# Kernel optimization log

Measured on AMD Instinct MI355X. Metric: run time of the kernel, lower is better.

The kernel has to match this reference:

```python
import jax, jax.numpy as jnp
import numpy as np

B, C, H, W = 4, 128, 64, 64
CQ = C // 8  # query/key channels = 16


def setup_inputs() -> dict:
    key = jax.random.key(0)
    ks = jax.random.split(key, 8)
    s = 0.05
    return {
        "x": jax.random.normal(ks[0], (B, C, H, W), jnp.float32),
        "wq": jax.random.normal(ks[1], (CQ, C), jnp.float32) * s,
        "bq": jax.random.normal(ks[2], (CQ,), jnp.float32) * s,
        "wk": jax.random.normal(ks[3], (CQ, C), jnp.float32) * s,
        "bk": jax.random.normal(ks[4], (CQ,), jnp.float32) * s,
        "wv": jax.random.normal(ks[5], (C, C), jnp.float32) * s,
        "bv": jax.random.normal(ks[6], (C,), jnp.float32) * s,
        # original inits gamma to 0; use small nonzero so attention path is exercised
        "gamma": jax.random.normal(ks[7], (1,), jnp.float32) * 0.1,
    }


def reference(x, wq, bq, wk, bk, wv, bv, gamma):
    b, c, h, w = x.shape
    n = h * w
    xf = x.reshape(b, c, n)  # [B, C, N]
    # 1x1 convs are per-position linear maps over channels
    q = jnp.einsum("qc,bcn->bnq", wq, xf) + bq            # [B, N, Cq]
    k = jnp.einsum("qc,bcn->bqn", wk, xf) + bk[:, None]   # [B, Cq, N]
    v = jnp.einsum("oc,bcn->bon", wv, xf) + bv[:, None]   # [B, C, N]
    # unscaled scores, softmax over keys (last dim), as in the original
    attn = jax.nn.softmax(jnp.einsum("bnq,bqm->bnm", q, k), axis=-1)  # [B, N, N]
    # out = value @ attention^T : out[b,c,n] = sum_m v[b,c,m] * attn[b,n,m]
    out = jnp.einsum("bom,bnm->bon", v, attn)             # [B, C, N]
    return gamma[0] * out.reshape(b, c, h, w) + x
```

## Files before the change

kernel.cpp:

```cpp
#include <hip/hip_runtime.h>
#include <hip/hip_bf16.h>

typedef float f32x4  __attribute__((ext_vector_type(4)));
typedef float f32x16 __attribute__((ext_vector_type(16)));
typedef short s16x8  __attribute__((ext_vector_type(8)));

#define NB 4
#define NC 128
#define NNPOS 4096
#define KSP 4
#define QBLK 128

__device__ __forceinline__ short bf16s(float x) {
    __hip_bfloat16 h = __float2bfloat16(x);
    return *reinterpret_cast<short*>(&h);
}
__device__ __forceinline__ int packbf2(float lo, float hi) {
    __hip_bfloat162 t = __float22bfloat162_rn(float2{lo, hi});
    return *reinterpret_cast<int*>(&t);
}
__device__ __forceinline__ float bf2f(unsigned short u) {
    unsigned int v = ((unsigned int)u) << 16;
    return *reinterpret_cast<float*>(&v);
}

__global__ __launch_bounds__(256) void qkv_kernel(
    const float* __restrict__ x,
    const float* __restrict__ wq, const float* __restrict__ bq,
    const float* __restrict__ wk, const float* __restrict__ bk,
    const float* __restrict__ wv, const float* __restrict__ bv,
    short* __restrict__ qb, short* __restrict__ kb, short* __restrict__ vt)
{
    const int n0  = blockIdx.x * 32;
    const int b   = blockIdx.y;
    const int tid = threadIdx.x;
    const int w = tid >> 6, lane = tid & 63, quad = lane >> 4, nn = lane & 15;

    __shared__ __align__(16) short xsT[32 * 136];

    #pragma unroll
    for (int p = 0; p < 4; ++p) {
        int idx = tid + p * 256;
        int cc = idx >> 3, n4 = (idx & 7) * 4;
        f32x4 xv = *(const f32x4*)&x[((size_t)(b * NC + cc)) * NNPOS + n0 + n4];
        #pragma unroll
        for (int j = 0; j < 4; ++j)
            xsT[(n4 + j) * 136 + cc] = bf16s(xv[j]);
    }

    s16x8 af[3][4];
    bool  live[3];
    f32x4 biasv[3];
    #pragma unroll
    for (int t = 0; t < 3; ++t) {
        int rid = 3 * w + t;
        int R   = rid * 16;
        const float* wsrc = nullptr; const float* bsrc = nullptr; int row0 = 0;
        if (rid < 8)        { wsrc = wv; bsrc = bv; row0 = R; }
        else if (rid == 8)  { wsrc = wq; bsrc = bq; row0 = 0; }
        else if (rid == 10) { wsrc = wk; bsrc = bk; row0 = 0; }
        live[t] = (wsrc != nullptr);
        #pragma unroll
        for (int r = 0; r < 4; ++r)
            biasv[t][r] = live[t] ? bsrc[row0 + quad * 4 + r] : 0.0f;
        if (live[t]) {
            #pragma unroll
            for (int ks = 0; ks < 4; ++ks) {
                const float* src = wsrc + (size_t)(row0 + nn) * NC + ks * 32 + quad * 8;
                f32x4 wa = *(const f32x4*)src;
                f32x4 wb = *(const f32x4*)(src + 4);
                s16x8 f;
                #pragma unroll
                for (int j = 0; j < 4; ++j) { f[j] = bf16s(wa[j]); f[j + 4] = bf16s(wb[j]); }
                af[t][ks] = f;
            }
        }
    }
    __syncthreads();

    f32x4 acc[3][2];
    #pragma unroll
    for (int t = 0; t < 3; ++t)
        #pragma unroll
        for (int nt = 0; nt < 2; ++nt)
            acc[t][nt] = biasv[t];

    #pragma unroll
    for (int nt = 0; nt < 2; ++nt) {
        s16x8 bf[4];
        #pragma unroll
        for (int ks = 0; ks < 4; ++ks)
            bf[ks] = *(const s16x8*)&xsT[(nt * 16 + nn) * 136 + ks * 32 + quad * 8];
        #pragma unroll
        for (int t = 0; t < 3; ++t)
            if (live[t])
                #pragma unroll
                for (int ks = 0; ks < 4; ++ks)
                    acc[t][nt] = __builtin_amdgcn_mfma_f32_16x16x32_bf16(af[t][ks], bf[ks], acc[t][nt], 0, 0, 0);
    }

    #pragma unroll
    for (int t = 0; t < 3; ++t) {
        if (!live[t]) continue;
        int R = (3 * w + t) * 16;
        #pragma unroll
        for (int nt = 0; nt < 2; ++nt) {
            int n = n0 + nt * 16 + nn;
            #pragma unroll
            for (int r = 0; r < 4; ++r) {
                short v = bf16s(acc[t][nt][r]);
                int row = R + quad * 4 + r;
                if (row < 128)
                    vt[((size_t)(b * NC + row)) * NNPOS + n] = v;
                else if (row < 144)
                    qb[((size_t)(b * NNPOS) + n) * 16 + (row - 128)] = v;
                else
                    kb[((size_t)(b * NNPOS) + n) * 16 + (row - 160)] = v;
            }
        }
    }
}

__global__ __launch_bounds__(256, 2) void attn_kernel(
    const short* __restrict__ qb, const short* __restrict__ kb,
    const short* __restrict__ vt,
    unsigned short* __restrict__ Ow, float* __restrict__ lw)
{
    const int qblk = blockIdx.x;
    const int s    = blockIdx.y;
    const int b    = blockIdx.z;
    const int tid  = threadIdx.x;
    const int w = tid >> 6, lane = tid & 63, h = lane >> 5, c31 = lane & 31;

    __shared__ __align__(16) short vts[128 * 72];

    const int q0 = qblk * QBLK + w * 32;

    s16x8 bq = *(const s16x8*)(qb + ((size_t)(b * NNPOS) + q0 + c31) * 16 + h * 8);

    f32x16 acc[4];
    #pragma unroll
    for (int ct = 0; ct < 4; ++ct)
        #pragma unroll
        for (int r = 0; r < 16; ++r) acc[ct][r] = 0.0f;
    float lp = 0.0f;

    const int mbase = s * (NNPOS / KSP);

    for (int it = 0; it < (NNPOS / KSP) / 64; ++it) {
        const int m0 = mbase + it * 64;

        s16x8 ak0 = *(const s16x8*)(kb + ((size_t)(b * NNPOS) + m0      + c31) * 16 + h * 8);
        s16x8 ak1 = *(const s16x8*)(kb + ((size_t)(b * NNPOS) + m0 + 32 + c31) * 16 + h * 8);

        __syncthreads();
        #pragma unroll
        for (int p = 0; p < 4; ++p) {
            int idx = tid + p * 256;
            int cc = idx >> 3, jq = idx & 7;
            *(uint4*)(vts + cc * 72 + jq * 8) =
                *(const uint4*)(vt + ((size_t)(b * NC + cc)) * NNPOS + m0 + jq * 8);
        }

        f32x16 z;
        #pragma unroll
        for (int r = 0; r < 16; ++r) z[r] = 0.0f;
        f32x16 s0 = __builtin_amdgcn_mfma_f32_32x32x16_bf16(ak0, bq, z, 0, 0, 0);
        f32x16 s1 = __builtin_amdgcn_mfma_f32_32x32x16_bf16(ak1, bq, z, 0, 0, 0);

        int d[16];
        #pragma unroll
        for (int i = 0; i < 8; ++i) {
            float p0 = __expf(fminf(s0[2 * i], 80.f));
            float p1 = __expf(fminf(s0[2 * i + 1], 80.f));
            lp += p0 + p1;
            d[i] = packbf2(p0, p1);
        }
        #pragma unroll
        for (int i = 0; i < 8; ++i) {
            float p0 = __expf(fminf(s1[2 * i], 80.f));
            float p1 = __expf(fminf(s1[2 * i + 1], 80.f));
            lp += p0 + p1;
            d[8 + i] = packbf2(p0, p1);
        }
        int xw[16];
        #pragma unroll
        for (int i = 0; i < 16; ++i) xw[i] = __shfl_xor(d[i], 32, 64);

        s16x8 pa[4];
        #pragma unroll
        for (int kp = 0; kp < 4; ++kp) {
            int e = kp * 4;
            union { int i[4]; s16x8 v; } u;
            u.i[0] = h ? xw[e + 2] : d[e];
            u.i[1] = h ? xw[e + 3] : d[e + 1];
            u.i[2] = h ? d[e + 2]  : xw[e];
            u.i[3] = h ? d[e + 3]  : xw[e + 1];
            pa[kp] = u.v;
        }

        __syncthreads();
        #pragma unroll
        for (int kp = 0; kp < 4; ++kp)
            #pragma unroll
            for (int ct = 0; ct < 4; ++ct) {
                s16x8 bv = *(const s16x8*)(vts + (ct * 32 + c31) * 72 + kp * 16 + h * 8);
                acc[ct] = __builtin_amdgcn_mfma_f32_32x32x16_bf16(pa[kp], bv, acc[ct], 0, 0, 0);
            }
    }

    lp += __shfl_xor(lp, 32, 64);
    if (lane < 32)
        lw[((size_t)(b * KSP + s)) * NNPOS + q0 + c31] = lp;

    #pragma unroll
    for (int ct = 0; ct < 4; ++ct)
        #pragma unroll
        for (int r = 0; r < 16; ++r) {
            int q = q0 + (r & 3) + 8 * (r >> 2) + 4 * h;
            Ow[(((size_t)(b * KSP + s)) * NNPOS + q) * NC + ct * 32 + c31] =
                (unsigned short)bf16s(acc[ct][r]);
        }
}

__global__ __launch_bounds__(256) void combine_kernel(
    const unsigned short* __restrict__ Ow, const float* __restrict__ lw,
    const float* __restrict__ x, const float* __restrict__ gamma,
    float* __restrict__ out)
{
    const int n0  = blockIdx.x * 64;
    const int b   = blockIdx.y;
    const int tid = threadIdx.x;

    __shared__ float ot[128 * 65 + 64];
    float* lsum = ot + 128 * 65;

    if (tid < 64) {
        float sl = 0.f;
        #pragma unroll
        for (int sI = 0; sI < KSP; ++sI)
            sl += lw[((size_t)(b * KSP + sI)) * NNPOS + n0 + tid];
        lsum[tid] = sl;
    }
    __syncthreads();

    #pragma unroll
    for (int p = 0; p < 16; ++p) {
        int e = tid + p * 256;
        int cp = e & 63, n = e >> 6;
        float a0 = 0.f, a1 = 0.f;
        #pragma unroll
        for (int sI = 0; sI < KSP; ++sI) {
            const unsigned short* src = Ow +
                (((size_t)(b * KSP + sI)) * NNPOS + n0 + n) * NC + cp * 2;
            ushort2 u = *(const ushort2*)src;
            a0 += bf2f(u.x);
            a1 += bf2f(u.y);
        }
        float inv = 1.0f / lsum[n];
        ot[(cp * 2) * 65 + n]     = a0 * inv;
        ot[(cp * 2 + 1) * 65 + n] = a1 * inv;
    }
    __syncthreads();

    const float g = gamma[0];
    #pragma unroll
    for (int p = 0; p < 32; ++p) {
        int e = tid + p * 256;
        int n = e & 63, c = e >> 6;
        size_t a = ((size_t)(b * NC + c)) * NNPOS + n0 + n;
        out[a] = g * ot[c * 65 + n] + x[a];
    }
}

extern "C" void kernel_launch(void* const* d_in, const int* in_sizes, int n_in,
                              void* d_out, int out_size, void* d_ws, size_t ws_size,
                              hipStream_t stream) {
    const float* x     = (const float*)d_in[0];
    const float* wq    = (const float*)d_in[1];
    const float* bq    = (const float*)d_in[2];
    const float* wk    = (const float*)d_in[3];
    const float* bk    = (const float*)d_in[4];
    const float* wv    = (const float*)d_in[5];
    const float* bv    = (const float*)d_in[6];
    const float* gamma = (const float*)d_in[7];
    float* out = (float*)d_out;

    short* qb = (short*)d_ws;
    short* kb = qb + (size_t)NB * NNPOS * 16;
    short* vt = kb + (size_t)NB * NNPOS * 16;
    unsigned short* Ow = (unsigned short*)(vt + (size_t)NB * NC * NNPOS);
    float* lw = (float*)(Ow + (size_t)NB * KSP * NNPOS * NC);

    qkv_kernel<<<dim3(128, NB), 256, 0, stream>>>(x, wq, bq, wk, bk, wv, bv, qb, kb, vt);
    attn_kernel<<<dim3(NNPOS / QBLK, KSP, NB), 256, 0, stream>>>(qb, kb, vt, Ow, lw);
    combine_kernel<<<dim3(NNPOS / 64, NB), 256, 0, stream>>>(Ow, lw, x, gamma, out);
}
```

Baseline: 122.3 us.

## Register-tile two query tiles per wave and load V directly from global

The attention kernel now has each wave handle 64 queries as two 32-row tiles, so every V fragment feeds two MFMAs. The shared-memory staging of V and both block barriers are removed, and V fragments are read straight from global memory into registers in two halves. The key-split count doubles and the query block doubles, which keeps the grid size the same but doubles the partial outputs the combine kernel must read. Accumulator register pressure doubles, which may cut occupancy or cause spills.

```diff
diff --git a/kernel.cpp b/kernel.cpp
--- a/kernel.cpp
+++ b/kernel.cpp
@@ -8,8 +8,8 @@
 #define NB 4
 #define NC 128
 #define NNPOS 4096
-#define KSP 4
-#define QBLK 128
+#define KSP 8
+#define QBLK 256
 
 __device__ __forceinline__ short bf16s(float x) {
     __hip_bfloat16 h = __float2bfloat16(x);
@@ -132,20 +132,22 @@
     const int tid  = threadIdx.x;
     const int w = tid >> 6, lane = tid & 63, h = lane >> 5, c31 = lane & 31;
 
-    __shared__ __align__(16) short vts[128 * 72];
-
-    const int q0 = qblk * QBLK + w * 32;
-
-    s16x8 bq = *(const s16x8*)(qb + ((size_t)(b * NNPOS) + q0 + c31) * 16 + h * 8);
-
-    f32x16 acc[4];
-    #pragma unroll
-    for (int ct = 0; ct < 4; ++ct)
-        #pragma unroll
-        for (int r = 0; r < 16; ++r) acc[ct][r] = 0.0f;
-    float lp = 0.0f;
+    const int q0 = qblk * QBLK + w * 64;
+
+    s16x8 bq0 = *(const s16x8*)(qb + ((size_t)(b * NNPOS) + q0      + c31) * 16 + h * 8);
+    s16x8 bq1 = *(const s16x8*)(qb + ((size_t)(b * NNPOS) + q0 + 32 + c31) * 16 + h * 8);
+
+    f32x16 acc[2][4];
+    #pragma unroll
+    for (int qt = 0; qt < 2; ++qt)
+        #pragma unroll
+        for (int ct = 0; ct < 4; ++ct)
+            #pragma unroll
+            for (int r = 0; r < 16; ++r) acc[qt][ct][r] = 0.0f;
+    float lp[2] = {0.f, 0.f};
 
     const int mbase = s * (NNPOS / KSP);
+    const short* vbase = vt + (size_t)(b * NC) * NNPOS;
 
     for (int it = 0; it < (NNPOS / KSP) / 64; ++it) {
         const int m0 = mbase + it * 64;
@@ -153,74 +155,96 @@
         s16x8 ak0 = *(const s16x8*)(kb + ((size_t)(b * NNPOS) + m0      + c31) * 16 + h * 8);
         s16x8 ak1 = *(const s16x8*)(kb + ((size_t)(b * NNPOS) + m0 + 32 + c31) * 16 + h * 8);
 
-        __syncthreads();
-        #pragma unroll
-        for (int p = 0; p < 4; ++p) {
-            int idx = tid + p * 256;
-            int cc = idx >> 3, jq = idx & 7;
-            *(uint4*)(vts + cc * 72 + jq * 8) =
-                *(const uint4*)(vt + ((size_t)(b * NC + cc)) * NNPOS + m0 + jq * 8);
+        s16x8 vb0[4][2];
+        #pragma unroll
+        for (int ct = 0; ct < 4; ++ct)
+            #pragma unroll
+            for (int k2 = 0; k2 < 2; ++k2)
+                vb0[ct][k2] = *(const s16x8*)(vbase +
+                    (size_t)(ct * 32 + c31) * NNPOS + m0 + k2 * 16 + h * 8);
+
+        s16x8 pa[2][4];
+        #pragma unroll
+        for (int qt = 0; qt < 2; ++qt) {
+            s16x8 bqt = qt ? bq1 : bq0;
+            f32x16 z;
+            #pragma unroll
+            for (int r = 0; r < 16; ++r) z[r] = 0.0f;
+            f32x16 s0 = __builtin_amdgcn_mfma_f32_32x32x16_bf16(ak0, bqt, z, 0, 0, 0);
+            f32x16 s1 = __builtin_amdgcn_mfma_f32_32x32x16_bf16(ak1, bqt, z, 0, 0, 0);
+            int d[16];
+            #pragma unroll
+            for (int i = 0; i < 8; ++i) {
+                float p0 = __expf(fminf(s0[2 * i], 80.f));
+                float p1 = __expf(fminf(s0[2 * i + 1], 80.f));
+                lp[qt] += p0 + p1;
+                d[i] = packbf2(p0, p1);
+            }
+            #pragma unroll
+            for (int i = 0; i < 8; ++i) {
+                float p0 = __expf(fminf(s1[2 * i], 80.f));
+                float p1 = __expf(fminf(s1[2 * i + 1], 80.f));
+                lp[qt] += p0 + p1;
+                d[8 + i] = packbf2(p0, p1);
+            }
+            int xw[16];
+            #pragma unroll
+            for (int i = 0; i < 16; ++i) xw[i] = __shfl_xor(d[i], 32, 64);
+            #pragma unroll
+            for (int kp = 0; kp < 4; ++kp) {
+                int e = kp * 4;
+                union { int i[4]; s16x8 v; } u;
+                u.i[0] = h ? xw[e + 2] : d[e];
+                u.i[1] = h ? xw[e + 3] : d[e + 1];
+                u.i[2] = h ? d[e + 2]  : xw[e];
+                u.i[3] = h ? d[e + 3]  : xw[e + 1];
+                pa[qt][kp] = u.v;
+            }
         }
 
-        f32x16 z;
-        #pragma unroll
-        for (int r = 0; r < 16; ++r) z[r] = 0.0f;
-        f32x16 s0 = __builtin_amdgcn_mfma_f32_32x32x16_bf16(ak0, bq, z, 0, 0, 0);
-        f32x16 s1 = __builtin_amdgcn_mfma_f32_32x32x16_bf16(ak1, bq, z, 0, 0, 0);
-
-        int d[16];
-        #pragma unroll
-        for (int i = 0; i < 8; ++i) {
-            float p0 = __expf(fminf(s0[2 * i], 80.f));
-            float p1 = __expf(fminf(s0[2 * i + 1], 80.f));
-            lp += p0 + p1;
-            d[i] = packbf2(p0, p1);
-        }
-        #pragma unroll
-        for (int i = 0; i < 8; ++i) {
-            float p0 = __expf(fminf(s1[2 * i], 80.f));
-            float p1 = __expf(fminf(s1[2 * i + 1], 80.f));
-            lp += p0 + p1;
-            d[8 + i] = packbf2(p0, p1);
-        }
-        int xw[16];
-        #pragma unroll
-        for (int i = 0; i < 16; ++i) xw[i] = __shfl_xor(d[i], 32, 64);
-
-        s16x8 pa[4];
-        #pragma unroll
-        for (int kp = 0; kp < 4; ++kp) {
-            int e = kp * 4;
-            union { int i[4]; s16x8 v; } u;
-            u.i[0] = h ? xw[e + 2] : d[e];
-            u.i[1] = h ? xw[e + 3] : d[e + 1];
-            u.i[2] = h ? d[e + 2]  : xw[e];
-            u.i[3] = h ? d[e + 3]  : xw[e + 1];
-            pa[kp] = u.v;
-        }
-
-        __syncthreads();
-        #pragma unroll
-        for (int kp = 0; kp < 4; ++kp)
-            #pragma unroll
-            for (int ct = 0; ct < 4; ++ct) {
-                s16x8 bv = *(const s16x8*)(vts + (ct * 32 + c31) * 72 + kp * 16 + h * 8);
-                acc[ct] = __builtin_amdgcn_mfma_f32_32x32x16_bf16(pa[kp], bv, acc[ct], 0, 0, 0);
-            }
-    }
-
-    lp += __shfl_xor(lp, 32, 64);
-    if (lane < 32)
-        lw[((size_t)(b * KSP + s)) * NNPOS + q0 + c31] = lp;
-
-    #pragma unroll
-    for (int ct = 0; ct < 4; ++ct)
-        #pragma unroll
-        for (int r = 0; r < 16; ++r) {
-            int q = q0 + (r & 3) + 8 * (r >> 2) + 4 * h;
-            Ow[(((size_t)(b * KSP + s)) * NNPOS + q) * NC + ct * 32 + c31] =
-                (unsigned short)bf16s(acc[ct][r]);
-        }
+        #pragma unroll
+        for (int ct = 0; ct < 4; ++ct)
+            #pragma unroll
+            for (int k2 = 0; k2 < 2; ++k2)
+                #pragma unroll
+                for (int qt = 0; qt < 2; ++qt)
+                    acc[qt][ct] = __builtin_amdgcn_mfma_f32_32x32x16_bf16(
+                        pa[qt][k2], vb0[ct][k2], acc[qt][ct], 0, 0, 0);
+
+        s16x8 vb1[4][2];
+        #pragma unroll
+        for (int ct = 0; ct < 4; ++ct)
+            #pragma unroll
+            for (int k2 = 0; k2 < 2; ++k2)
+                vb1[ct][k2] = *(const s16x8*)(vbase +
+                    (size_t)(ct * 32 + c31) * NNPOS + m0 + (2 + k2) * 16 + h * 8);
+        #pragma unroll
+        for (int ct = 0; ct < 4; ++ct)
+            #pragma unroll
+            for (int k2 = 0; k2 < 2; ++k2)
+                #pragma unroll
+                for (int qt = 0; qt < 2; ++qt)
+                    acc[qt][ct] = __builtin_amdgcn_mfma_f32_32x32x16_bf16(
+                        pa[qt][2 + k2], vb1[ct][k2], acc[qt][ct], 0, 0, 0);
+    }
+
+    #pragma unroll
+    for (int qt = 0; qt < 2; ++qt) {
+        lp[qt] += __shfl_xor(lp[qt], 32, 64);
+        if (lane < 32)
+            lw[((size_t)(b * KSP + s)) * NNPOS + q0 + qt * 32 + c31] = lp[qt];
+    }
+
+    #pragma unroll
+    for (int qt = 0; qt < 2; ++qt)
+        #pragma unroll
+        for (int ct = 0; ct < 4; ++ct)
+            #pragma unroll
+            for (int r = 0; r < 16; ++r) {
+                int q = q0 + qt * 32 + (r & 3) + 8 * (r >> 2) + 4 * h;
+                Ow[(((size_t)(b * KSP + s)) * NNPOS + q) * NC + ct * 32 + c31] =
+                    (unsigned short)bf16s(acc[qt][ct][r]);
+            }
 }
 
 __global__ __launch_bounds__(256) void combine_kernel(
```

Measured after the change: 133.8 us. 1.09x slower.

## Pre-tile V for direct MFMA loads, drop LDS staging, use exp2 with folded log2e

Applied to the files above, without the earlier changes.

The QKV kernel now writes V in a tiled layout that matches the MFMA B-operand fragment, so the attention kernel loads V fragments straight from global memory into registers. This removes the LDS staging and both barriers per iteration. The key split count doubles to 8, the grid is reordered so key-split blocks sit next to each other, and log2(e) is folded into Wq/bq so the softmax can use a raw exp2 instruction. The costs are that each wave now does its own redundant global V loads (relying on L2) and the combine kernel has to read twice as many partial outputs.

```diff
diff --git a/kernel.cpp b/kernel.cpp
--- a/kernel.cpp
+++ b/kernel.cpp
@@ -8,8 +8,8 @@
 #define NB 4
 #define NC 128
 #define NNPOS 4096
-#define KSP 4
-#define QBLK 128
+#define KSP 8
+#define LOG2E 1.44269504088896f
 
 __device__ __forceinline__ short bf16s(float x) {
     __hip_bfloat16 h = __float2bfloat16(x);
@@ -22,6 +22,9 @@
 __device__ __forceinline__ float bf2f(unsigned short u) {
     unsigned int v = ((unsigned int)u) << 16;
     return *reinterpret_cast<float*>(&v);
+}
+__device__ __forceinline__ float exp2fast(float x) {
+    return __builtin_amdgcn_exp2f(x);
 }
 
 __global__ __launch_bounds__(256) void qkv_kernel(
@@ -56,13 +59,14 @@
         int rid = 3 * w + t;
         int R   = rid * 16;
         const float* wsrc = nullptr; const float* bsrc = nullptr; int row0 = 0;
+        float scale = 1.0f;
         if (rid < 8)        { wsrc = wv; bsrc = bv; row0 = R; }
-        else if (rid == 8)  { wsrc = wq; bsrc = bq; row0 = 0; }
+        else if (rid == 8)  { wsrc = wq; bsrc = bq; row0 = 0; scale = LOG2E; }
         else if (rid == 10) { wsrc = wk; bsrc = bk; row0 = 0; }
         live[t] = (wsrc != nullptr);
         #pragma unroll
         for (int r = 0; r < 4; ++r)
-            biasv[t][r] = live[t] ? bsrc[row0 + quad * 4 + r] : 0.0f;
+            biasv[t][r] = live[t] ? scale * bsrc[row0 + quad * 4 + r] : 0.0f;
         if (live[t]) {
             #pragma unroll
             for (int ks = 0; ks < 4; ++ks) {
@@ -71,7 +75,10 @@
                 f32x4 wb = *(const f32x4*)(src + 4);
                 s16x8 f;
                 #pragma unroll
-                for (int j = 0; j < 4; ++j) { f[j] = bf16s(wa[j]); f[j + 4] = bf16s(wb[j]); }
+                for (int j = 0; j < 4; ++j) {
+                    f[j]     = bf16s(scale * wa[j]);
+                    f[j + 4] = bf16s(scale * wb[j]);
+                }
                 af[t][ks] = f;
             }
         }
@@ -106,13 +113,15 @@
         #pragma unroll
         for (int nt = 0; nt < 2; ++nt) {
             int n = n0 + nt * 16 + nn;
+            int kg = (n0 + nt * 16) >> 4;
             #pragma unroll
             for (int r = 0; r < 4; ++r) {
                 short v = bf16s(acc[t][nt][r]);
                 int row = R + quad * 4 + r;
-                if (row < 128)
-                    vt[((size_t)(b * NC + row)) * NNPOS + n] = v;
-                else if (row < 144)
+                if (row < 128) {
+                    int ct = row >> 5, c31r = row & 31;
+                    vt[((((size_t)b * 256 + kg) * 4 + ct) * 32 + c31r) * 16 + nn] = v;
+                } else if (row < 144)
                     qb[((size_t)(b * NNPOS) + n) * 16 + (row - 128)] = v;
                 else
                     kb[((size_t)(b * NNPOS) + n) * 16 + (row - 160)] = v;
@@ -126,15 +135,13 @@
     const short* __restrict__ vt,
     unsigned short* __restrict__ Ow, float* __restrict__ lw)
 {
-    const int qblk = blockIdx.x;
-    const int s    = blockIdx.y;
-    const int b    = blockIdx.z;
-    const int tid  = threadIdx.x;
+    const int s   = blockIdx.x;
+    const int b   = blockIdx.z;
+    const int tid = threadIdx.x;
     const int w = tid >> 6, lane = tid & 63, h = lane >> 5, c31 = lane & 31;
 
-    __shared__ __align__(16) short vts[128 * 72];
-
-    const int q0 = qblk * QBLK + w * 32;
+    const int qt = blockIdx.y * 4 + w;
+    const int q0 = qt * 32;
 
     s16x8 bq = *(const s16x8*)(qb + ((size_t)(b * NNPOS) + q0 + c31) * 16 + h * 8);
 
@@ -145,22 +152,26 @@
         for (int r = 0; r < 16; ++r) acc[ct][r] = 0.0f;
     float lp = 0.0f;
 
+    const short* kbp = kb + (size_t)(b * NNPOS) * 16;
+    const short* vbp = vt + (size_t)b * (256 * 4 * 512);
     const int mbase = s * (NNPOS / KSP);
-
+    const int kgbase = mbase >> 4;
+
+    #pragma unroll 2
     for (int it = 0; it < (NNPOS / KSP) / 64; ++it) {
         const int m0 = mbase + it * 64;
-
-        s16x8 ak0 = *(const s16x8*)(kb + ((size_t)(b * NNPOS) + m0      + c31) * 16 + h * 8);
-        s16x8 ak1 = *(const s16x8*)(kb + ((size_t)(b * NNPOS) + m0 + 32 + c31) * 16 + h * 8);
-
-        __syncthreads();
-        #pragma unroll
-        for (int p = 0; p < 4; ++p) {
-            int idx = tid + p * 256;
-            int cc = idx >> 3, jq = idx & 7;
-            *(uint4*)(vts + cc * 72 + jq * 8) =
-                *(const uint4*)(vt + ((size_t)(b * NC + cc)) * NNPOS + m0 + jq * 8);
-        }
+        const int kg0 = kgbase + it * 4;
+
+        s16x8 ak0 = *(const s16x8*)(kbp + (size_t)(m0      + c31) * 16 + h * 8);
+        s16x8 ak1 = *(const s16x8*)(kbp + (size_t)(m0 + 32 + c31) * 16 + h * 8);
+
+        s16x8 vb[4][4];
+        #pragma unroll
+        for (int kp = 0; kp < 4; ++kp)
+            #pragma unroll
+            for (int ct = 0; ct < 4; ++ct)
+                vb[kp][ct] = *(const s16x8*)(vbp +
+                    (((size_t)(kg0 + kp) * 4 + ct) << 9) + (c31 << 4) + (h << 3));
 
         f32x16 z;
         #pragma unroll
@@ -171,15 +182,15 @@
         int d[16];
         #pragma unroll
         for (int i = 0; i < 8; ++i) {
-            float p0 = __expf(fminf(s0[2 * i], 80.f));
-            float p1 = __expf(fminf(s0[2 * i + 1], 80.f));
+            float p0 = exp2fast(fminf(s0[2 * i], 126.f));
+            float p1 = exp2fast(fminf(s0[2 * i + 1], 126.f));
             lp += p0 + p1;
             d[i] = packbf2(p0, p1);
         }
         #pragma unroll
         for (int i = 0; i < 8; ++i) {
-            float p0 = __expf(fminf(s1[2 * i], 80.f));
-            float p1 = __expf(fminf(s1[2 * i + 1], 80.f));
+            float p0 = exp2fast(fminf(s1[2 * i], 126.f));
+            float p1 = exp2fast(fminf(s1[2 * i + 1], 126.f));
             lp += p0 + p1;
             d[8 + i] = packbf2(p0, p1);
         }
@@ -199,14 +210,12 @@
             pa[kp] = u.v;
         }
 
-        __syncthreads();
         #pragma unroll
         for (int kp = 0; kp < 4; ++kp)
             #pragma unroll
-            for (int ct = 0; ct < 4; ++ct) {
-                s16x8 bv = *(const s16x8*)(vts + (ct * 32 + c31) * 72 + kp * 16 + h * 8);
-                acc[ct] = __builtin_amdgcn_mfma_f32_32x32x16_bf16(pa[kp], bv, acc[ct], 0, 0, 0);
-            }
+            for (int ct = 0; ct < 4; ++ct)
+                acc[ct] = __builtin_amdgcn_mfma_f32_32x32x16_bf16(
+                    pa[kp], vb[kp][ct], acc[ct], 0, 0, 0);
     }
 
     lp += __shfl_xor(lp, 32, 64);
@@ -293,6 +302,6 @@
     float* lw = (float*)(Ow + (size_t)NB * KSP * NNPOS * NC);
 
     qkv_kernel<<<dim3(128, NB), 256, 0, stream>>>(x, wq, bq, wk, bk, wv, bv, qb, kb, vt);
-    attn_kernel<<<dim3(NNPOS / QBLK, KSP, NB), 256, 0, stream>>>(qb, kb, vt, Ow, lw);
+    attn_kernel<<<dim3(KSP, 32, NB), 256, 0, stream>>>(qb, kb, vt, Ow, lw);
     combine_kernel<<<dim3(NNPOS / 64, NB), 256, 0, stream>>>(Ow, lw, x, gamma, out);
 }
```

New measurement: 127.0 us. +3.9%, slower.
